# Kernel tuning notes

Hardware: AMD Instinct MI355X
Metric: run time of the kernel (lower is better)

## Reference

```python
import jax, jax.numpy as jnp
import numpy as np

B = 64           # batch size
N = 512          # number of nodes
E = 1            # edge feature dims of the GSO
M = 256          # nodes carrying edge-variant weights (hybrid EV since M < N)
F = [1, 8, 8]    # node-signal features per layer
K = [3, 3]       # shift taps per layer
MLP = [512, 128] # readout dims
P_EDGE = 0.03    # graph density
ZTOL = 1e-9      # zero tolerance for sparsity pattern


def setup_inputs():
    ks = jax.random.split(jax.random.key(0), 13)
    x = jax.random.normal(ks[0], (B, F[0], N), dtype=jnp.float32)
    adj = (jax.random.uniform(ks[1], (E, N, N)) < P_EDGE).astype(jnp.float32)
    S = adj * jax.random.normal(ks[2], (E, N, N), dtype=jnp.float32) / np.sqrt(N * P_EDGE)

    def w(k, shape, scale):
        return jax.random.normal(k, shape, dtype=jnp.float32) * np.float32(scale)

    wEV1 = w(ks[3], (F[1], E, K[0], F[0], N, N), 1.0 / np.sqrt(F[0] * N))
    wLSI1 = w(ks[4], (F[1], E, K[0], F[0]), 1.0 / np.sqrt(F[0] * K[0]))
    b1 = w(ks[5], (F[1], 1), 0.1)
    wEV2 = w(ks[6], (F[2], E, K[1], F[1], N, N), 1.0 / np.sqrt(F[1] * N))
    wLSI2 = w(ks[7], (F[2], E, K[1], F[1]), 1.0 / np.sqrt(F[1] * K[1]))
    b2 = w(ks[8], (F[2], 1), 0.1)
    W1 = w(ks[9], (MLP[0], F[2] * N), 1.0 / np.sqrt(F[2] * N))
    bW1 = w(ks[10], (MLP[0],), 0.1)
    W2 = w(ks[11], (MLP[1], MLP[0]), 1.0 / np.sqrt(MLP[0]))
    bW2 = w(ks[12], (MLP[1],), 0.1)
    return dict(x=x, S=S, wEV1=wEV1, wLSI1=wLSI1, b1=b1,
                wEV2=wEV2, wLSI2=wLSI2, b2=b2, W1=W1, bW1=bW1, W2=W2, bW2=bW2)


def _sparsity_mask(S):
    # support of S + I, then kill the [M:, M:] block (hybrid EV mask)
    eye = jnp.eye(N, dtype=S.dtype)
    sp = ((jnp.abs(S) + eye[None]) > ZTOL).astype(S.dtype)      # (E,N,N)
    hyb = jnp.ones((N, N), S.dtype).at[M:, M:].set(0.0)
    return sp * hyb[None]


def _ev_layer(xl, S, sp, wEV, wLSI, b):
    # xl: (B,G,N); wEV: (F,E,K,G,N,N); wLSI: (F,E,K,G); b: (F,1)
    Phi = wEV * sp[None, :, None, None]                          # masked filter matrices
    Kl = wEV.shape[2]
    # EV part: y = sum_k Phi^(k) ... Phi^(0) x, summed over e, g
    z = jnp.einsum('fegmn,bgn->bfegm', Phi[:, :, 0], xl)
    y = z
    for k in range(1, Kl):
        z = jnp.einsum('fegmn,bfegn->bfegm', Phi[:, :, k], z)
        y = y + z
    y = y.sum(axis=(2, 3))                                       # (B,F,N)
    # LSI part of the hybrid filter: sum_{e,k,g} h_{fekg} S_e^k x_g
    xe = jnp.broadcast_to(xl[:, None], (xl.shape[0], S.shape[0]) + xl.shape[1:])
    zs = [xe]                                                    # k = 0: identity
    for k in range(1, Kl):
        zs.append(jnp.einsum('emn,begn->begm', S, zs[-1]))
    zst = jnp.stack(zs, axis=2)                                  # (B,E,K,G,N)
    y = y + jnp.einsum('fekg,bekgn->bfn', wLSI, zst)
    return y + b[None]                                           # bias broadcast over nodes


def reference(x, S, wEV1, wLSI1, b1, wEV2, wLSI2, b2, W1, bW1, W2, bW2):
    sp = _sparsity_mask(S)
    # order=None -> permIdentity, so x[:, :, order] == x; NoPool is identity
    y = _ev_layer(x, S, sp, wEV1, wLSI1, b1)
    y = _ev_layer(y, S, sp, wEV2, wLSI2, b2)
    yf = y.reshape(y.shape[0], -1)                               # (B, F[-1]*N)
    h = yf @ W1.T + bW1                                          # linear MLP (no activation)
    return h @ W2.T + bW2
```

## Files before the change

kernel.cpp:

```cpp
#include <hip/hip_runtime.h>
#include <cstdint>
#include <cstddef>

#define NNODE 512
#define MMASK 256
#define ZT 1e-9f
#define NPL 216

__global__ __launch_bounds__(256) void k_prep(const float* __restrict__ x,
                                              const float* __restrict__ S,
                                              int* __restrict__ sp_col, int* __restrict__ sp_cnt,
                                              int* __restrict__ s_col, float* __restrict__ s_val,
                                              int* __restrict__ s_cnt,
                                              float* __restrict__ xt) {
  int gtid = blockIdx.x * 256 + threadIdx.x;
  int W = gtid >> 6, lane = threadIdx.x & 63;
  {
    int n = gtid >> 6, b = gtid & 63;
    xt[gtid] = x[b * NNODE + n];
  }
  int m = W;
  int csp = 0, cs = 0;
  unsigned long long lt = (1ull << lane) - 1ull;
  for (int ch = 0; ch < 8; ++ch) {
    int n = ch * 64 + lane;
    float s = S[m * NNODE + n];
    bool ps  = (s != 0.f);
    bool psp = ((fabsf(s) + ((m == n) ? 1.f : 0.f)) > ZT) && !((m >= MMASK) && (n >= MMASK));
    unsigned long long msp = __ballot(psp), ms = __ballot(ps);
    if (psp) { int p = csp + __popcll(msp & lt); if (p < 64) sp_col[(m << 6) + p] = n; }
    if (ps)  { int p = cs  + __popcll(ms  & lt); if (p < 64) { s_col[(m << 6) + p] = n; s_val[(m << 6) + p] = s; } }
    csp += __popcll(msp); cs += __popcll(ms);
  }
  if (lane >= csp) sp_col[(m << 6) + lane] = 0;
  if (lane >= cs)  { s_col[(m << 6) + lane] = 0; s_val[(m << 6) + lane] = 0.f; }
  if (lane == 0) { sp_cnt[m] = (csp < 64 ? csp : 64); s_cnt[m] = (cs < 64 ? cs : 64); }
}

__global__ __launch_bounds__(256) void k_pack(const float* __restrict__ wEV1,
                                              const float* __restrict__ wEV2,
                                              const int* __restrict__ sp_col,
                                              const int* __restrict__ sp_cnt,
                                              float* __restrict__ wpk) {
  __shared__ float rowbuf[4][512];
  int wv = threadIdx.x >> 6, lane = threadIdx.x & 63;
  int W = __builtin_amdgcn_readfirstlane(blockIdx.x * 4 + wv);
  int nwv = gridDim.x * 4;
  for (int job = W; job < NPL * NNODE; job += nwv) {
    int p = job >> 9, r = job & 511;
    const float* src = ((p < 24) ? (wEV1 + ((size_t)p << 18))
                                 : (wEV2 + ((size_t)(p - 24) << 18))) + (r << 9);
    float4 a = ((const float4*)src)[lane];
    float4 b = ((const float4*)src)[64 + lane];
    ((float4*)rowbuf[wv])[lane] = a;
    ((float4*)rowbuf[wv])[64 + lane] = b;
    int cl = sp_col[(r << 6) + lane];
    float wl = (lane < sp_cnt[r]) ? rowbuf[wv][cl] : 0.f;
    wpk[((size_t)p << 15) + (r << 6) + lane] = wl;
  }
}

__device__ __forceinline__ float ell_mac_s(const int* __restrict__ cols,
                                           const float* __restrict__ ws,
                                           int cnt,
                                           const float* __restrict__ zin, int lane) {
  float a0 = 0.f, a1 = 0.f, a2 = 0.f, a3 = 0.f;
  for (int base = 0; base < cnt; base += 16) {
#pragma unroll
    for (int i = 0; i < 16; i += 4) {
      int   c0 = cols[base + i    ]; float w0 = ws[base + i    ];
      int   c1 = cols[base + i + 1]; float w1 = ws[base + i + 1];
      int   c2 = cols[base + i + 2]; float w2 = ws[base + i + 2];
      int   c3 = cols[base + i + 3]; float w3 = ws[base + i + 3];
      a0 += w0 * zin[(c0 << 6) + lane];
      a1 += w1 * zin[(c1 << 6) + lane];
      a2 += w2 * zin[(c2 << 6) + lane];
      a3 += w3 * zin[(c3 << 6) + lane];
    }
  }
  return (a0 + a1) + (a2 + a3);
}

__global__ __launch_bounds__(256) void k_l1s0(const float* __restrict__ wpk,
    const int* __restrict__ sp_col, const int* __restrict__ sp_cnt,
    const int* __restrict__ s_col, const float* __restrict__ s_val, const int* __restrict__ s_cnt,
    const float* __restrict__ xt, float* __restrict__ zA1, float* __restrict__ u1) {
  int lane = threadIdx.x & 63;
  int W = __builtin_amdgcn_readfirstlane((blockIdx.x * 256 + (int)threadIdx.x) >> 6);
  int nwv = (gridDim.x << 2);
  for (int u = W; u < 4608; u += nwv) {
    if (u < 4096) {
      int f = u >> 9, r = u & 511;
      zA1[((size_t)f << 15) + (r << 6) + lane] =
          ell_mac_s(sp_col + (r << 6), wpk + ((size_t)(f * 3 + 0) << 15) + (r << 6),
                    sp_cnt[r], xt, lane);
    } else {
      int r = u - 4096;
      u1[(r << 6) + lane] =
          ell_mac_s(s_col + (r << 6), s_val + (r << 6), s_cnt[r], xt, lane);
    }
  }
}

__global__ __launch_bounds__(256) void k_l1s1(const float* __restrict__ wpk,
    const int* __restrict__ sp_col, const int* __restrict__ sp_cnt,
    const int* __restrict__ s_col, const float* __restrict__ s_val, const int* __restrict__ s_cnt,
    const float* __restrict__ zA1, const float* __restrict__ u1,
    float* __restrict__ zB1, float* __restrict__ u2) {
  int lane = threadIdx.x & 63;
  int W = __builtin_amdgcn_readfirstlane((blockIdx.x * 256 + (int)threadIdx.x) >> 6);
  int nwv = (gridDim.x << 2);
  for (int u = W; u < 4608; u += nwv) {
    if (u < 4096) {
      int f = u >> 9, r = u & 511;
      zB1[((size_t)f << 15) + (r << 6) + lane] =
          ell_mac_s(sp_col + (r << 6), wpk + ((size_t)(f * 3 + 1) << 15) + (r << 6),
                    sp_cnt[r], zA1 + ((size_t)f << 15), lane);
    } else {
      int r = u - 4096;
      u2[(r << 6) + lane] =
          ell_mac_s(s_col + (r << 6), s_val + (r << 6), s_cnt[r], u1, lane);
    }
  }
}

__global__ __launch_bounds__(256) void k_l1s2(const float* __restrict__ wpk,
    const int* __restrict__ sp_col, const int* __restrict__ sp_cnt,
    const float* __restrict__ zA1, const float* __restrict__ zB1,
    const float* __restrict__ xt, const float* __restrict__ u1, const float* __restrict__ u2,
    const float* __restrict__ wLSI1, const float* __restrict__ b1, float* __restrict__ y1) {
  int lane = threadIdx.x & 63;
  int W = __builtin_amdgcn_readfirstlane((blockIdx.x * 256 + (int)threadIdx.x) >> 6);
  int nwv = (gridDim.x << 2);
  for (int u = W; u < 4096; u += nwv) {
    int f = u >> 9, r = u & 511;
    float a = ell_mac_s(sp_col + (r << 6), wpk + ((size_t)(f * 3 + 2) << 15) + (r << 6),
                        sp_cnt[r], zB1 + ((size_t)f << 15), lane);
    int idx = (r << 6) + lane;
    size_t fi = ((size_t)f << 15) + idx;
    y1[fi] = zA1[fi] + zB1[fi] + a
           + wLSI1[f * 3 + 0] * xt[idx] + wLSI1[f * 3 + 1] * u1[idx]
           + wLSI1[f * 3 + 2] * u2[idx] + b1[f];
  }
}

__global__ __launch_bounds__(256) void k_l2s0(const float* __restrict__ wpk,
    const int* __restrict__ sp_col, const int* __restrict__ sp_cnt,
    const int* __restrict__ s_col, const float* __restrict__ s_val, const int* __restrict__ s_cnt,
    const float* __restrict__ y1, float* __restrict__ zA2, float* __restrict__ v1) {
  int lane = threadIdx.x & 63;
  int W = __builtin_amdgcn_readfirstlane((blockIdx.x * 256 + (int)threadIdx.x) >> 6);
  int nwv = (gridDim.x << 2);
  for (int u = W; u < 36864; u += nwv) {
    if (u < 32768) {
      int c = u >> 9, r = u & 511;
      int f = c >> 3, g = c & 7;
      zA2[((size_t)c << 15) + (r << 6) + lane] =
          ell_mac_s(sp_col + (r << 6),
                    wpk + ((size_t)(24 + (f * 3 + 0) * 8 + g) << 15) + (r << 6),
                    sp_cnt[r], y1 + ((size_t)g << 15), lane);
    } else {
      int t = u - 32768;
      int g = t >> 9, r = t & 511;
      v1[((size_t)g << 15) + (r << 6) + lane] =
          ell_mac_s(s_col + (r << 6), s_val + (r << 6), s_cnt[r],
                    y1 + ((size_t)g << 15), lane);
    }
  }
}

__global__ __launch_bounds__(256) void k_l2s1(const float* __restrict__ wpk,
    const int* __restrict__ sp_col, const int* __restrict__ sp_cnt,
    const int* __restrict__ s_col, const float* __restrict__ s_val, const int* __restrict__ s_cnt,
    const float* __restrict__ zA2, const float* __restrict__ v1,
    float* __restrict__ zB2, float* __restrict__ v2) {
  int lane = threadIdx.x & 63;
  int W = __builtin_amdgcn_readfirstlane((blockIdx.x * 256 + (int)threadIdx.x) >> 6);
  int nwv = (gridDim.x << 2);
  for (int u = W; u < 36864; u += nwv) {
    if (u < 32768) {
      int c = u >> 9, r = u & 511;
      int f = c >> 3, g = c & 7;
      zB2[((size_t)c << 15) + (r << 6) + lane] =
          ell_mac_s(sp_col + (r << 6),
                    wpk + ((size_t)(24 + (f * 3 + 1) * 8 + g) << 15) + (r << 6),
                    sp_cnt[r], zA2 + ((size_t)c << 15), lane);
    } else {
      int t = u - 32768;
      int g = t >> 9, r = t & 511;
      v2[((size_t)g << 15) + (r << 6) + lane] =
          ell_mac_s(s_col + (r << 6), s_val + (r << 6), s_cnt[r],
                    v1 + ((size_t)g << 15), lane);
    }
  }
}

__global__ __launch_bounds__(256) void k_l2s2(const float* __restrict__ wpk,
    const int* __restrict__ sp_col, const int* __restrict__ sp_cnt,
    const float* __restrict__ zA2, const float* __restrict__ zB2,
    const float* __restrict__ y1, const float* __restrict__ v1, const float* __restrict__ v2,
    const float* __restrict__ wLSI2, const float* __restrict__ b2,
    const float* __restrict__ bW1, float* __restrict__ y2, float* __restrict__ ht) {
  int gtid = blockIdx.x * 256 + threadIdx.x;
  int lane = threadIdx.x & 63;
  int W = __builtin_amdgcn_readfirstlane(gtid >> 6);
  int nwv = (gridDim.x << 2);
  if (gtid < 32768) ht[gtid] = bW1[gtid >> 6];
  for (int u = W; u < 4096; u += nwv) {
    int f = u >> 9, r = u & 511;
    int idx = (r << 6) + lane;
    const int* cols = sp_col + (r << 6);
    int cnt = sp_cnt[r];
    float acc = b2[f];
#pragma unroll
    for (int g = 0; g < 8; ++g) {
      int c = f * 8 + g;
      float a = ell_mac_s(cols,
                          wpk + ((size_t)(24 + (f * 3 + 2) * 8 + g) << 15) + (r << 6),
                          cnt, zB2 + ((size_t)c << 15), lane);
      size_t ci = ((size_t)c << 15) + idx;
      size_t gi = ((size_t)g << 15) + idx;
      acc += zA2[ci] + zB2[ci] + a
           + wLSI2[f * 24 + g]      * y1[gi]
           + wLSI2[f * 24 + 8 + g]  * v1[gi]
           + wLSI2[f * 24 + 16 + g] * v2[gi];
    }
    y2[((size_t)f << 15) + idx] = acc;
  }
}

__global__ __launch_bounds__(256) void k_gemm1(const float* __restrict__ W1,
                                               const float* __restrict__ y2,
                                               const float* __restrict__ bW2,
                                               float* __restrict__ ht,
                                               float* __restrict__ out) {
  int gtid = blockIdx.x * 256 + threadIdx.x;
  int lane = threadIdx.x & 63;
  int W = __builtin_amdgcn_readfirstlane(gtid >> 6);
  int nwv = (gridDim.x << 2);
  if (gtid < 8192) out[gtid] = bW2[gtid & 127];
  for (int u = W; u < 2048; u += nwv) {
    int pg = u >> 5, qs = u & 31;
    const float* wrow = W1 + (size_t)pg * 8 * 4096 + qs * 128;
    const float* yb = y2 + ((size_t)(qs * 128) << 6);
    float acc[8] = {0, 0, 0, 0, 0, 0, 0, 0};
    for (int q = 0; q < 128; q += 8) {
      float yv[8];
#pragma unroll
      for (int i = 0; i < 8; ++i) yv[i] = yb[((q + i) << 6) + lane];
#pragma unroll
      for (int i = 0; i < 8; ++i) {
#pragma unroll
        for (int p = 0; p < 8; ++p) acc[p] += wrow[(size_t)p * 4096 + q + i] * yv[i];
      }
    }
#pragma unroll
    for (int p = 0; p < 8; ++p) atomicAdd(&ht[((pg * 8 + p) << 6) + lane], acc[p]);
  }
}

__global__ __launch_bounds__(256) void k_gemm2(const float* __restrict__ W2,
                                               const float* __restrict__ ht,
                                               float* __restrict__ out) {
  int lane = threadIdx.x & 63;
  int W = __builtin_amdgcn_readfirstlane((blockIdx.x * 256 + (int)threadIdx.x) >> 6);
  int nwv = (gridDim.x << 2);
  for (int u = W; u < 1024; u += nwv) {
    int o = u >> 3, qs = u & 7;
    const float* w2 = W2 + (size_t)o * 512 + qs * 64;
    const float* hb = ht + ((size_t)(qs * 64) << 6);
    float acc = 0.f;
    for (int q = 0; q < 64; q += 8) {
#pragma unroll
      for (int i = 0; i < 8; ++i) acc += w2[q + i] * hb[((q + i) << 6) + lane];
    }
    atomicAdd(&out[lane * 128 + o], acc);
  }
}

extern "C" void kernel_launch(void* const* d_in, const int* in_sizes, int n_in,
                              void* d_out, int out_size, void* d_ws, size_t ws_size,
                              hipStream_t stream) {
  const float* x     = (const float*)d_in[0];
  const float* S     = (const float*)d_in[1];
  const float* wEV1  = (const float*)d_in[2];
  const float* wLSI1 = (const float*)d_in[3];
  const float* b1    = (const float*)d_in[4];
  const float* wEV2  = (const float*)d_in[5];
  const float* wLSI2 = (const float*)d_in[6];
  const float* b2    = (const float*)d_in[7];
  const float* W1    = (const float*)d_in[8];
  const float* bW1   = (const float*)d_in[9];
  const float* W2    = (const float*)d_in[10];
  const float* bW2   = (const float*)d_in[11];
  float* out = (float*)d_out;

  char* w = (char*)d_ws;
  auto alloc = [&](size_t bytes) { char* p = w; w += (bytes + 255) & ~(size_t)255; return p; };
  int*   sp_col = (int*)alloc(512 * 64 * 4);
  int*   sp_cnt = (int*)alloc(512 * 4);
  int*   s_col  = (int*)alloc(512 * 64 * 4);
  float* s_val  = (float*)alloc(512 * 64 * 4);
  int*   s_cnt  = (int*)alloc(512 * 4);
  float* wpk    = (float*)alloc((size_t)NPL * 32768 * 4);
  float* xt     = (float*)alloc((size_t)32768 * 4);
  float* u1     = (float*)alloc((size_t)32768 * 4);
  float* u2     = (float*)alloc((size_t)32768 * 4);
  float* zA1    = (float*)alloc((size_t)8 * 32768 * 4);
  float* zB1    = (float*)alloc((size_t)8 * 32768 * 4);
  float* y1     = (float*)alloc((size_t)8 * 32768 * 4);
  float* zA2    = (float*)alloc((size_t)64 * 32768 * 4);
  float* zB2    = (float*)alloc((size_t)64 * 32768 * 4);
  float* v1     = (float*)alloc((size_t)8 * 32768 * 4);
  float* v2     = (float*)alloc((size_t)8 * 32768 * 4);
  float* y2     = (float*)alloc((size_t)8 * 32768 * 4);
  float* ht     = (float*)alloc((size_t)32768 * 4);
  (void)ws_size; (void)in_sizes; (void)n_in; (void)out_size;

  k_prep<<<128, 256, 0, stream>>>(x, S, sp_col, sp_cnt, s_col, s_val, s_cnt, xt);
  k_pack<<<2048, 256, 0, stream>>>(wEV1, wEV2, sp_col, sp_cnt, wpk);
  k_l1s0<<<1152, 256, 0, stream>>>(wpk, sp_col, sp_cnt, s_col, s_val, s_cnt, xt, zA1, u1);
  k_l1s1<<<1152, 256, 0, stream>>>(wpk, sp_col, sp_cnt, s_col, s_val, s_cnt, zA1, u1, zB1, u2);
  k_l1s2<<<1024, 256, 0, stream>>>(wpk, sp_col, sp_cnt, zA1, zB1, xt, u1, u2, wLSI1, b1, y1);
  k_l2s0<<<9216, 256, 0, stream>>>(wpk, sp_col, sp_cnt, s_col, s_val, s_cnt, y1, zA2, v1);
  k_l2s1<<<9216, 256, 0, stream>>>(wpk, sp_col, sp_cnt, s_col, s_val, s_cnt, zA2, v1, zB2, v2);
  k_l2s2<<<1024, 256, 0, stream>>>(wpk, sp_col, sp_cnt, zA2, zB2, y1, v1, v2, wLSI2, b2, bW1, y2, ht);
  k_gemm1<<<512, 256, 0, stream>>>(W1, y2, bW2, ht, out);
  k_gemm2<<<256, 256, 0, stream>>>(W2, ht, out);
}
```

Baseline: 409.9 us.

## Gather edge-variant weights directly from dense tensors, removing the pack kernel

Removes the pre-pass that streamed the full dense wEV1/wEV2 tensors to build a packed ELL weight buffer. Each sparse MAC now loads only the weight entries at the row's nonzero columns, straight from the dense tensors. This avoids reading every dense weight and writing then re-reading the packed buffer. In exchange, the weight loads become scattered: each one may pull a whole cache line for a single float, and they sit on the critical path of every shift kernel. The k_l2s2 grid is also halved.

```diff
diff --git a/kernel.cpp b/kernel.cpp
--- a/kernel.cpp
+++ b/kernel.cpp
@@ -5,7 +5,6 @@
 #define NNODE 512
 #define MMASK 256
 #define ZT 1e-9f
-#define NPL 216
 
 __global__ __launch_bounds__(256) void k_prep(const float* __restrict__ x,
                                               const float* __restrict__ S,
@@ -37,27 +36,27 @@
   if (lane == 0) { sp_cnt[m] = (csp < 64 ? csp : 64); s_cnt[m] = (cs < 64 ? cs : 64); }
 }
 
-__global__ __launch_bounds__(256) void k_pack(const float* __restrict__ wEV1,
-                                              const float* __restrict__ wEV2,
-                                              const int* __restrict__ sp_col,
-                                              const int* __restrict__ sp_cnt,
-                                              float* __restrict__ wpk) {
-  __shared__ float rowbuf[4][512];
-  int wv = threadIdx.x >> 6, lane = threadIdx.x & 63;
-  int W = __builtin_amdgcn_readfirstlane(blockIdx.x * 4 + wv);
-  int nwv = gridDim.x * 4;
-  for (int job = W; job < NPL * NNODE; job += nwv) {
-    int p = job >> 9, r = job & 511;
-    const float* src = ((p < 24) ? (wEV1 + ((size_t)p << 18))
-                                 : (wEV2 + ((size_t)(p - 24) << 18))) + (r << 9);
-    float4 a = ((const float4*)src)[lane];
-    float4 b = ((const float4*)src)[64 + lane];
-    ((float4*)rowbuf[wv])[lane] = a;
-    ((float4*)rowbuf[wv])[64 + lane] = b;
-    int cl = sp_col[(r << 6) + lane];
-    float wl = (lane < sp_cnt[r]) ? rowbuf[wv][cl] : 0.f;
-    wpk[((size_t)p << 15) + (r << 6) + lane] = wl;
-  }
+__device__ __forceinline__ float ell_mac_gd(const int* __restrict__ cols,
+                                            const float* __restrict__ wrow,
+                                            int cnt,
+                                            const float* __restrict__ zin, int lane) {
+  float a0 = 0.f, a1 = 0.f, a2 = 0.f, a3 = 0.f;
+  for (int base = 0; base < cnt; base += 8) {
+#pragma unroll
+    for (int i = 0; i < 8; i += 4) {
+      int j = base + i;
+      int c0 = cols[j], c1 = cols[j + 1], c2 = cols[j + 2], c3 = cols[j + 3];
+      float w0 = wrow[c0]; w0 = (j     < cnt) ? w0 : 0.f;
+      float w1 = wrow[c1]; w1 = (j + 1 < cnt) ? w1 : 0.f;
+      float w2 = wrow[c2]; w2 = (j + 2 < cnt) ? w2 : 0.f;
+      float w3 = wrow[c3]; w3 = (j + 3 < cnt) ? w3 : 0.f;
+      a0 += w0 * zin[(c0 << 6) + lane];
+      a1 += w1 * zin[(c1 << 6) + lane];
+      a2 += w2 * zin[(c2 << 6) + lane];
+      a3 += w3 * zin[(c3 << 6) + lane];
+    }
+  }
+  return (a0 + a1) + (a2 + a3);
 }
 
 __device__ __forceinline__ float ell_mac_s(const int* __restrict__ cols,
@@ -81,7 +80,7 @@
   return (a0 + a1) + (a2 + a3);
 }
 
-__global__ __launch_bounds__(256) void k_l1s0(const float* __restrict__ wpk,
+__global__ __launch_bounds__(256) void k_l1s0(const float* __restrict__ wEV1,
     const int* __restrict__ sp_col, const int* __restrict__ sp_cnt,
     const int* __restrict__ s_col, const float* __restrict__ s_val, const int* __restrict__ s_cnt,
     const float* __restrict__ xt, float* __restrict__ zA1, float* __restrict__ u1) {
@@ -92,8 +91,8 @@
     if (u < 4096) {
       int f = u >> 9, r = u & 511;
       zA1[((size_t)f << 15) + (r << 6) + lane] =
-          ell_mac_s(sp_col + (r << 6), wpk + ((size_t)(f * 3 + 0) << 15) + (r << 6),
-                    sp_cnt[r], xt, lane);
+          ell_mac_gd(sp_col + (r << 6), wEV1 + ((size_t)(f * 3 + 0) << 18) + (r << 9),
+                     sp_cnt[r], xt, lane);
     } else {
       int r = u - 4096;
       u1[(r << 6) + lane] =
@@ -102,7 +101,7 @@
   }
 }
 
-__global__ __launch_bounds__(256) void k_l1s1(const float* __restrict__ wpk,
+__global__ __launch_bounds__(256) void k_l1s1(const float* __restrict__ wEV1,
     const int* __restrict__ sp_col, const int* __restrict__ sp_cnt,
     const int* __restrict__ s_col, const float* __restrict__ s_val, const int* __restrict__ s_cnt,
     const float* __restrict__ zA1, const float* __restrict__ u1,
@@ -114,8 +113,8 @@
     if (u < 4096) {
       int f = u >> 9, r = u & 511;
       zB1[((size_t)f << 15) + (r << 6) + lane] =
-          ell_mac_s(sp_col + (r << 6), wpk + ((size_t)(f * 3 + 1) << 15) + (r << 6),
-                    sp_cnt[r], zA1 + ((size_t)f << 15), lane);
+          ell_mac_gd(sp_col + (r << 6), wEV1 + ((size_t)(f * 3 + 1) << 18) + (r << 9),
+                     sp_cnt[r], zA1 + ((size_t)f << 15), lane);
     } else {
       int r = u - 4096;
       u2[(r << 6) + lane] =
@@ -124,7 +123,7 @@
   }
 }
 
-__global__ __launch_bounds__(256) void k_l1s2(const float* __restrict__ wpk,
+__global__ __launch_bounds__(256) void k_l1s2(const float* __restrict__ wEV1,
     const int* __restrict__ sp_col, const int* __restrict__ sp_cnt,
     const float* __restrict__ zA1, const float* __restrict__ zB1,
     const float* __restrict__ xt, const float* __restrict__ u1, const float* __restrict__ u2,
@@ -134,8 +133,8 @@
   int nwv = (gridDim.x << 2);
   for (int u = W; u < 4096; u += nwv) {
     int f = u >> 9, r = u & 511;
-    float a = ell_mac_s(sp_col + (r << 6), wpk + ((size_t)(f * 3 + 2) << 15) + (r << 6),
-                        sp_cnt[r], zB1 + ((size_t)f << 15), lane);
+    float a = ell_mac_gd(sp_col + (r << 6), wEV1 + ((size_t)(f * 3 + 2) << 18) + (r << 9),
+                         sp_cnt[r], zB1 + ((size_t)f << 15), lane);
     int idx = (r << 6) + lane;
     size_t fi = ((size_t)f << 15) + idx;
     y1[fi] = zA1[fi] + zB1[fi] + a
@@ -144,7 +143,7 @@
   }
 }
 
-__global__ __launch_bounds__(256) void k_l2s0(const float* __restrict__ wpk,
+__global__ __launch_bounds__(256) void k_l2s0(const float* __restrict__ wEV2,
     const int* __restrict__ sp_col, const int* __restrict__ sp_cnt,
     const int* __restrict__ s_col, const float* __restrict__ s_val, const int* __restrict__ s_cnt,
     const float* __restrict__ y1, float* __restrict__ zA2, float* __restrict__ v1) {
@@ -156,9 +155,9 @@
       int c = u >> 9, r = u & 511;
       int f = c >> 3, g = c & 7;
       zA2[((size_t)c << 15) + (r << 6) + lane] =
-          ell_mac_s(sp_col + (r << 6),
-                    wpk + ((size_t)(24 + (f * 3 + 0) * 8 + g) << 15) + (r << 6),
-                    sp_cnt[r], y1 + ((size_t)g << 15), lane);
+          ell_mac_gd(sp_col + (r << 6),
+                     wEV2 + ((size_t)((f * 3 + 0) * 8 + g) << 18) + (r << 9),
+                     sp_cnt[r], y1 + ((size_t)g << 15), lane);
     } else {
       int t = u - 32768;
       int g = t >> 9, r = t & 511;
@@ -169,7 +168,7 @@
   }
 }
 
-__global__ __launch_bounds__(256) void k_l2s1(const float* __restrict__ wpk,
+__global__ __launch_bounds__(256) void k_l2s1(const float* __restrict__ wEV2,
     const int* __restrict__ sp_col, const int* __restrict__ sp_cnt,
     const int* __restrict__ s_col, const float* __restrict__ s_val, const int* __restrict__ s_cnt,
     const float* __restrict__ zA2, const float* __restrict__ v1,
@@ -182,9 +181,9 @@
       int c = u >> 9, r = u & 511;
       int f = c >> 3, g = c & 7;
       zB2[((size_t)c << 15) + (r << 6) + lane] =
-          ell_mac_s(sp_col + (r << 6),
-                    wpk + ((size_t)(24 + (f * 3 + 1) * 8 + g) << 15) + (r << 6),
-                    sp_cnt[r], zA2 + ((size_t)c << 15), lane);
+          ell_mac_gd(sp_col + (r << 6),
+                     wEV2 + ((size_t)((f * 3 + 1) * 8 + g) << 18) + (r << 9),
+                     sp_cnt[r], zA2 + ((size_t)c << 15), lane);
     } else {
       int t = u - 32768;
       int g = t >> 9, r = t & 511;
@@ -195,7 +194,7 @@
   }
 }
 
-__global__ __launch_bounds__(256) void k_l2s2(const float* __restrict__ wpk,
+__global__ __launch_bounds__(256) void k_l2s2(const float* __restrict__ wEV2,
     const int* __restrict__ sp_col, const int* __restrict__ sp_cnt,
     const float* __restrict__ zA2, const float* __restrict__ zB2,
     const float* __restrict__ y1, const float* __restrict__ v1, const float* __restrict__ v2,
@@ -215,9 +214,9 @@
 #pragma unroll
     for (int g = 0; g < 8; ++g) {
       int c = f * 8 + g;
-      float a = ell_mac_s(cols,
-                          wpk + ((size_t)(24 + (f * 3 + 2) * 8 + g) << 15) + (r << 6),
-                          cnt, zB2 + ((size_t)c << 15), lane);
+      float a = ell_mac_gd(cols,
+                           wEV2 + ((size_t)((f * 3 + 2) * 8 + g) << 18) + (r << 9),
+                           cnt, zB2 + ((size_t)c << 15), lane);
       size_t ci = ((size_t)c << 15) + idx;
       size_t gi = ((size_t)g << 15) + idx;
       acc += zA2[ci] + zB2[ci] + a
@@ -302,7 +301,6 @@
   int*   s_col  = (int*)alloc(512 * 64 * 4);
   float* s_val  = (float*)alloc(512 * 64 * 4);
   int*   s_cnt  = (int*)alloc(512 * 4);
-  float* wpk    = (float*)alloc((size_t)NPL * 32768 * 4);
   float* xt     = (float*)alloc((size_t)32768 * 4);
   float* u1     = (float*)alloc((size_t)32768 * 4);
   float* u2     = (float*)alloc((size_t)32768 * 4);
@@ -318,13 +316,12 @@
   (void)ws_size; (void)in_sizes; (void)n_in; (void)out_size;
 
   k_prep<<<128, 256, 0, stream>>>(x, S, sp_col, sp_cnt, s_col, s_val, s_cnt, xt);
-  k_pack<<<2048, 256, 0, stream>>>(wEV1, wEV2, sp_col, sp_cnt, wpk);
-  k_l1s0<<<1152, 256, 0, stream>>>(wpk, sp_col, sp_cnt, s_col, s_val, s_cnt, xt, zA1, u1);
-  k_l1s1<<<1152, 256, 0, stream>>>(wpk, sp_col, sp_cnt, s_col, s_val, s_cnt, zA1, u1, zB1, u2);
-  k_l1s2<<<1024, 256, 0, stream>>>(wpk, sp_col, sp_cnt, zA1, zB1, xt, u1, u2, wLSI1, b1, y1);
-  k_l2s0<<<9216, 256, 0, stream>>>(wpk, sp_col, sp_cnt, s_col, s_val, s_cnt, y1, zA2, v1);
-  k_l2s1<<<9216, 256, 0, stream>>>(wpk, sp_col, sp_cnt, s_col, s_val, s_cnt, zA2, v1, zB2, v2);
-  k_l2s2<<<1024, 256, 0, stream>>>(wpk, sp_col, sp_cnt, zA2, zB2, y1, v1, v2, wLSI2, b2, bW1, y2, ht);
+  k_l1s0<<<1152, 256, 0, stream>>>(wEV1, sp_col, sp_cnt, s_col, s_val, s_cnt, xt, zA1, u1);
+  k_l1s1<<<1152, 256, 0, stream>>>(wEV1, sp_col, sp_cnt, s_col, s_val, s_cnt, zA1, u1, zB1, u2);
+  k_l1s2<<<1024, 256, 0, stream>>>(wEV1, sp_col, sp_cnt, zA1, zB1, xt, u1, u2, wLSI1, b1, y1);
+  k_l2s0<<<9216, 256, 0, stream>>>(wEV2, sp_col, sp_cnt, s_col, s_val, s_cnt, y1, zA2, v1);
+  k_l2s1<<<9216, 256, 0, stream>>>(wEV2, sp_col, sp_cnt, s_col, s_val, s_cnt, zA2, v1, zB2, v2);
+  k_l2s2<<<512, 256, 0, stream>>>(wEV2, sp_col, sp_cnt, zA2, zB2, y1, v1, v2, wLSI2, b2, bW1, y2, ht);
   k_gemm1<<<512, 256, 0, stream>>>(W1, y2, bW2, ht, out);
   k_gemm2<<<256, 256, 0, stream>>>(W2, ht, out);
 }
```

After: 503.1 us. +22.7%, slower.

## Overlap layer-2 weight packing with layer-1 stages and gather packed weights directly

Applied to the files above, without the earlier changes.

Splits the weight-packing kernel so only the layer-1 weights are packed up front. The layer-2 weights are packed by extra waves appended to the three layer-1 kernels, so that work overlaps the small layer-1 sparse passes, which alone leave the GPU underused. The packing now gathers only the needed sparse columns straight from global memory instead of staging full rows in LDS. The first readout GEMM also uses longer K chunks per wave to cut the number of atomic adds, at the cost of fewer waves and less parallelism.

```diff
diff --git a/kernel.cpp b/kernel.cpp
--- a/kernel.cpp
+++ b/kernel.cpp
@@ -37,27 +37,15 @@
   if (lane == 0) { sp_cnt[m] = (csp < 64 ? csp : 64); s_cnt[m] = (cs < 64 ? cs : 64); }
 }
 
-__global__ __launch_bounds__(256) void k_pack(const float* __restrict__ wEV1,
-                                              const float* __restrict__ wEV2,
-                                              const int* __restrict__ sp_col,
-                                              const int* __restrict__ sp_cnt,
-                                              float* __restrict__ wpk) {
-  __shared__ float rowbuf[4][512];
-  int wv = threadIdx.x >> 6, lane = threadIdx.x & 63;
-  int W = __builtin_amdgcn_readfirstlane(blockIdx.x * 4 + wv);
-  int nwv = gridDim.x * 4;
-  for (int job = W; job < NPL * NNODE; job += nwv) {
-    int p = job >> 9, r = job & 511;
-    const float* src = ((p < 24) ? (wEV1 + ((size_t)p << 18))
-                                 : (wEV2 + ((size_t)(p - 24) << 18))) + (r << 9);
-    float4 a = ((const float4*)src)[lane];
-    float4 b = ((const float4*)src)[64 + lane];
-    ((float4*)rowbuf[wv])[lane] = a;
-    ((float4*)rowbuf[wv])[64 + lane] = b;
-    int cl = sp_col[(r << 6) + lane];
-    float wl = (lane < sp_cnt[r]) ? rowbuf[wv][cl] : 0.f;
-    wpk[((size_t)p << 15) + (r << 6) + lane] = wl;
-  }
+__device__ __forceinline__ void pack_one(const float* __restrict__ src,
+                                         const int* __restrict__ sp_col,
+                                         const int* __restrict__ sp_cnt,
+                                         float* __restrict__ wpk,
+                                         int pidx, int r, int lane) {
+  int cl = sp_col[(r << 6) + lane];
+  int cnt = sp_cnt[r];
+  float wl = (lane < cnt) ? src[cl] : 0.f;
+  wpk[((size_t)pidx << 15) + (r << 6) + lane] = wl;
 }
 
 __device__ __forceinline__ float ell_mac_s(const int* __restrict__ cols,
@@ -81,66 +69,102 @@
   return (a0 + a1) + (a2 + a3);
 }
 
-__global__ __launch_bounds__(256) void k_l1s0(const float* __restrict__ wpk,
+__global__ __launch_bounds__(256) void k_packA(const float* __restrict__ wEV1,
+                                               const int* __restrict__ sp_col,
+                                               const int* __restrict__ sp_cnt,
+                                               float* __restrict__ wpk) {
+  int lane = threadIdx.x & 63;
+  int W = __builtin_amdgcn_readfirstlane((blockIdx.x * 256 + (int)threadIdx.x) >> 6);
+  int nwv = (gridDim.x << 2);
+  for (int u = W; u < 24 * 512; u += nwv) {
+    int p = u >> 9, r = u & 511;
+    pack_one(wEV1 + ((size_t)p << 18) + (r << 9), sp_col, sp_cnt, wpk, p, r, lane);
+  }
+}
+
+__global__ __launch_bounds__(256) void k_l1s0(const float* __restrict__ wEV2,
+    const float* __restrict__ wpk,
     const int* __restrict__ sp_col, const int* __restrict__ sp_cnt,
     const int* __restrict__ s_col, const float* __restrict__ s_val, const int* __restrict__ s_cnt,
-    const float* __restrict__ xt, float* __restrict__ zA1, float* __restrict__ u1) {
-  int lane = threadIdx.x & 63;
-  int W = __builtin_amdgcn_readfirstlane((blockIdx.x * 256 + (int)threadIdx.x) >> 6);
-  int nwv = (gridDim.x << 2);
-  for (int u = W; u < 4608; u += nwv) {
+    const float* __restrict__ xt, float* __restrict__ zA1, float* __restrict__ u1,
+    float* __restrict__ wpk_out) {
+  int lane = threadIdx.x & 63;
+  int W = __builtin_amdgcn_readfirstlane((blockIdx.x * 256 + (int)threadIdx.x) >> 6);
+  int nwv = (gridDim.x << 2);
+  for (int u = W; u < 4608 + 32768; u += nwv) {
     if (u < 4096) {
       int f = u >> 9, r = u & 511;
       zA1[((size_t)f << 15) + (r << 6) + lane] =
           ell_mac_s(sp_col + (r << 6), wpk + ((size_t)(f * 3 + 0) << 15) + (r << 6),
                     sp_cnt[r], xt, lane);
-    } else {
+    } else if (u < 4608) {
       int r = u - 4096;
       u1[(r << 6) + lane] =
           ell_mac_s(s_col + (r << 6), s_val + (r << 6), s_cnt[r], xt, lane);
-    }
-  }
-}
-
-__global__ __launch_bounds__(256) void k_l1s1(const float* __restrict__ wpk,
+    } else {
+      int jj = u - 4608;
+      int p2 = jj >> 9, r = jj & 511;
+      pack_one(wEV2 + ((size_t)p2 << 18) + (r << 9), sp_col, sp_cnt,
+               wpk_out, 24 + p2, r, lane);
+    }
+  }
+}
+
+__global__ __launch_bounds__(256) void k_l1s1(const float* __restrict__ wEV2,
+    const float* __restrict__ wpk,
     const int* __restrict__ sp_col, const int* __restrict__ sp_cnt,
     const int* __restrict__ s_col, const float* __restrict__ s_val, const int* __restrict__ s_cnt,
     const float* __restrict__ zA1, const float* __restrict__ u1,
-    float* __restrict__ zB1, float* __restrict__ u2) {
-  int lane = threadIdx.x & 63;
-  int W = __builtin_amdgcn_readfirstlane((blockIdx.x * 256 + (int)threadIdx.x) >> 6);
-  int nwv = (gridDim.x << 2);
-  for (int u = W; u < 4608; u += nwv) {
+    float* __restrict__ zB1, float* __restrict__ u2,
+    float* __restrict__ wpk_out) {
+  int lane = threadIdx.x & 63;
+  int W = __builtin_amdgcn_readfirstlane((blockIdx.x * 256 + (int)threadIdx.x) >> 6);
+  int nwv = (gridDim.x << 2);
+  for (int u = W; u < 4608 + 32768; u += nwv) {
     if (u < 4096) {
       int f = u >> 9, r = u & 511;
       zB1[((size_t)f << 15) + (r << 6) + lane] =
           ell_mac_s(sp_col + (r << 6), wpk + ((size_t)(f * 3 + 1) << 15) + (r << 6),
                     sp_cnt[r], zA1 + ((size_t)f << 15), lane);
-    } else {
+    } else if (u < 4608) {
       int r = u - 4096;
       u2[(r << 6) + lane] =
           ell_mac_s(s_col + (r << 6), s_val + (r << 6), s_cnt[r], u1, lane);
-    }
-  }
-}
-
-__global__ __launch_bounds__(256) void k_l1s2(const float* __restrict__ wpk,
+    } else {
+      int jj = u - 4608 + 32768;
+      int p2 = jj >> 9, r = jj & 511;
+      pack_one(wEV2 + ((size_t)p2 << 18) + (r << 9), sp_col, sp_cnt,
+               wpk_out, 24 + p2, r, lane);
+    }
+  }
+}
+
+__global__ __launch_bounds__(256) void k_l1s2(const float* __restrict__ wEV2,
+    const float* __restrict__ wpk,
     const int* __restrict__ sp_col, const int* __restrict__ sp_cnt,
     const float* __restrict__ zA1, const float* __restrict__ zB1,
     const float* __restrict__ xt, const float* __restrict__ u1, const float* __restrict__ u2,
-    const float* __restrict__ wLSI1, const float* __restrict__ b1, float* __restrict__ y1) {
-  int lane = threadIdx.x & 63;
-  int W = __builtin_amdgcn_readfirstlane((blockIdx.x * 256 + (int)threadIdx.x) >> 6);
-  int nwv = (gridDim.x << 2);
-  for (int u = W; u < 4096; u += nwv) {
-    int f = u >> 9, r = u & 511;
-    float a = ell_mac_s(sp_col + (r << 6), wpk + ((size_t)(f * 3 + 2) << 15) + (r << 6),
-                        sp_cnt[r], zB1 + ((size_t)f << 15), lane);
-    int idx = (r << 6) + lane;
-    size_t fi = ((size_t)f << 15) + idx;
-    y1[fi] = zA1[fi] + zB1[fi] + a
-           + wLSI1[f * 3 + 0] * xt[idx] + wLSI1[f * 3 + 1] * u1[idx]
-           + wLSI1[f * 3 + 2] * u2[idx] + b1[f];
+    const float* __restrict__ wLSI1, const float* __restrict__ b1, float* __restrict__ y1,
+    float* __restrict__ wpk_out) {
+  int lane = threadIdx.x & 63;
+  int W = __builtin_amdgcn_readfirstlane((blockIdx.x * 256 + (int)threadIdx.x) >> 6);
+  int nwv = (gridDim.x << 2);
+  for (int u = W; u < 4096 + 32768; u += nwv) {
+    if (u < 4096) {
+      int f = u >> 9, r = u & 511;
+      float a = ell_mac_s(sp_col + (r << 6), wpk + ((size_t)(f * 3 + 2) << 15) + (r << 6),
+                          sp_cnt[r], zB1 + ((size_t)f << 15), lane);
+      int idx = (r << 6) + lane;
+      size_t fi = ((size_t)f << 15) + idx;
+      y1[fi] = zA1[fi] + zB1[fi] + a
+             + wLSI1[f * 3 + 0] * xt[idx] + wLSI1[f * 3 + 1] * u1[idx]
+             + wLSI1[f * 3 + 2] * u2[idx] + b1[f];
+    } else {
+      int jj = u - 4096 + 65536;
+      int p2 = jj >> 9, r = jj & 511;
+      pack_one(wEV2 + ((size_t)p2 << 18) + (r << 9), sp_col, sp_cnt,
+               wpk_out, 24 + p2, r, lane);
+    }
   }
 }
 
@@ -239,12 +263,12 @@
   int W = __builtin_amdgcn_readfirstlane(gtid >> 6);
   int nwv = (gridDim.x << 2);
   if (gtid < 8192) out[gtid] = bW2[gtid & 127];
-  for (int u = W; u < 2048; u += nwv) {
-    int pg = u >> 5, qs = u & 31;
-    const float* wrow = W1 + (size_t)pg * 8 * 4096 + qs * 128;
-    const float* yb = y2 + ((size_t)(qs * 128) << 6);
+  for (int u = W; u < 512; u += nwv) {
+    int pg = u >> 3, ks = u & 7;
+    const float* wrow = W1 + (size_t)pg * 8 * 4096 + ks * 512;
+    const float* yb = y2 + ((size_t)(ks * 512) << 6);
     float acc[8] = {0, 0, 0, 0, 0, 0, 0, 0};
-    for (int q = 0; q < 128; q += 8) {
+    for (int q = 0; q < 512; q += 8) {
       float yv[8];
 #pragma unroll
       for (int i = 0; i < 8; ++i) yv[i] = yb[((q + i) << 6) + lane];
@@ -318,13 +342,13 @@
   (void)ws_size; (void)in_sizes; (void)n_in; (void)out_size;
 
   k_prep<<<128, 256, 0, stream>>>(x, S, sp_col, sp_cnt, s_col, s_val, s_cnt, xt);
-  k_pack<<<2048, 256, 0, stream>>>(wEV1, wEV2, sp_col, sp_cnt, wpk);
-  k_l1s0<<<1152, 256, 0, stream>>>(wpk, sp_col, sp_cnt, s_col, s_val, s_cnt, xt, zA1, u1);
-  k_l1s1<<<1152, 256, 0, stream>>>(wpk, sp_col, sp_cnt, s_col, s_val, s_cnt, zA1, u1, zB1, u2);
-  k_l1s2<<<1024, 256, 0, stream>>>(wpk, sp_col, sp_cnt, zA1, zB1, xt, u1, u2, wLSI1, b1, y1);
+  k_packA<<<3072, 256, 0, stream>>>(wEV1, sp_col, sp_cnt, wpk);
+  k_l1s0<<<9344, 256, 0, stream>>>(wEV2, wpk, sp_col, sp_cnt, s_col, s_val, s_cnt, xt, zA1, u1, wpk);
+  k_l1s1<<<9344, 256, 0, stream>>>(wEV2, wpk, sp_col, sp_cnt, s_col, s_val, s_cnt, zA1, u1, zB1, u2, wpk);
+  k_l1s2<<<9216, 256, 0, stream>>>(wEV2, wpk, sp_col, sp_cnt, zA1, zB1, xt, u1, u2, wLSI1, b1, y1, wpk);
   k_l2s0<<<9216, 256, 0, stream>>>(wpk, sp_col, sp_cnt, s_col, s_val, s_cnt, y1, zA2, v1);
   k_l2s1<<<9216, 256, 0, stream>>>(wpk, sp_col, sp_cnt, s_col, s_val, s_cnt, zA2, v1, zB2, v2);
   k_l2s2<<<1024, 256, 0, stream>>>(wpk, sp_col, sp_cnt, zA2, zB2, y1, v1, v2, wLSI2, b2, bW1, y2, ht);
-  k_gemm1<<<512, 256, 0, stream>>>(W1, y2, bW2, ht, out);
+  k_gemm1<<<128, 256, 0, stream>>>(W1, y2, bW2, ht, out);
   k_gemm2<<<256, 256, 0, stream>>>(W2, ht, out);
 }
```

New measurement: 396.6 us. 1.03x faster.
